# Kernel optimization log

Measured on AMD Instinct MI355X. Metric: run time of the kernel, lower is better.

Reference implementation:

```python
import jax, jax.numpy as jnp
import numpy as np

B, T = 4, 2048
IN_H, OUT_H = 4096, 4096   # in_hidden_size = output features, out_hidden_size = input features (torch F.linear quirk)
RANK = 1024


def setup_inputs() -> dict:
    key = jax.random.key(0)
    kx, ku, ks, kv, kb = jax.random.split(key, 5)
    x = jax.random.normal(kx, (B, T, OUT_H), dtype=jnp.float32)
    U = jax.random.normal(ku, (IN_H, RANK), dtype=jnp.float32) * 0.02
    S = jax.random.uniform(ks, (RANK,), dtype=jnp.float32)
    V = jax.random.normal(kv, (OUT_H, RANK), dtype=jnp.float32) * 0.02
    bias = jax.random.normal(kb, (IN_H,), dtype=jnp.float32) * 0.01
    return {"x": x, "U": U, "S": S, "V": V, "bias": bias}


def reference(x, U, S, V, bias):
    # Faithful to torch: M = U @ diag(S) @ V.T  (shape [in_hidden, out_hidden]);
    # F.linear(x, M, bias) = x @ M.T + bias, so x:[...,out_hidden] -> out:[...,in_hidden]
    M = (U * S) @ V.T                     # [IN_H, OUT_H]; (U*S) == U @ diag(S)
    return jnp.einsum('bto,io->bti', x, M) + bias
```

## Files before the change

### kernel.cpp

```cpp
#include <hip/hip_runtime.h>
#include <stdint.h>

typedef __attribute__((ext_vector_type(4))) float  floatx4;
typedef __attribute__((ext_vector_type(8))) short  short8;
typedef __attribute__((ext_vector_type(8))) __bf16 bf16x8;

__device__ __forceinline__ unsigned short f2bf(float f) {
  unsigned int u = __builtin_bit_cast(unsigned int, f);
  u += 0x7fffu + ((u >> 16) & 1u);
  return (unsigned short)(u >> 16);
}

typedef const __attribute__((address_space(1))) void* gptr_t;
typedef __attribute__((address_space(3))) void*       lptr_t;

__global__ __launch_bounds__(256) void prep_fused(
    const float* __restrict__ X, const float* __restrict__ V,
    const float* __restrict__ U, const float* __restrict__ S,
    unsigned short* __restrict__ Xb, unsigned short* __restrict__ Vt,
    unsigned short* __restrict__ Ub,
    int castBlocks, int transTotal, int transGX, int vrows, int vcols,
    unsigned int rankMask) {
  __shared__ float tile[32][33];
  int bid = blockIdx.x;
  int tid = threadIdx.x;
  if (bid < castBlocks) {
    size_t i = ((size_t)bid * 256 + tid) * 8;
    const floatx4* p = (const floatx4*)(X + i);
    floatx4 a = p[0], b = p[1];
    union { unsigned short us[8]; short8 v; } o;
    o.us[0] = f2bf(a[0]); o.us[1] = f2bf(a[1]); o.us[2] = f2bf(a[2]); o.us[3] = f2bf(a[3]);
    o.us[4] = f2bf(b[0]); o.us[5] = f2bf(b[1]); o.us[6] = f2bf(b[2]); o.us[7] = f2bf(b[3]);
    *(short8*)(Xb + i) = o.v;
  } else if (bid < castBlocks + transTotal) {
    int b  = bid - castBlocks;
    int bx = (b % transGX) * 32;
    int by = (b / transGX) * 32;
    int tx = tid & 31;
    int ty = tid >> 5;
    for (int i = ty; i < 32; i += 8)
      tile[i][tx] = V[(size_t)(by + i) * vcols + bx + tx];
    __syncthreads();
    for (int i = ty; i < 32; i += 8)
      Vt[(size_t)(bx + i) * vrows + by + tx] = f2bf(tile[tx][i]);
  } else {
    int b = bid - castBlocks - transTotal;
    size_t i = ((size_t)b * 256 + tid) * 4;
    floatx4 u = *(const floatx4*)(U + i);
    floatx4 s = *(const floatx4*)(S + (i & (size_t)rankMask));
    union { unsigned short us[4]; unsigned long long v; } o;
    o.us[0] = f2bf(u[0] * s[0]); o.us[1] = f2bf(u[1] * s[1]);
    o.us[2] = f2bf(u[2] * s[2]); o.us[3] = f2bf(u[3] * s[3]);
    *(unsigned long long*)(Ub + i) = o.v;
  }
}

__global__ __launch_bounds__(256, 2)
void gemm1_kernel(const unsigned short* __restrict__ A,
                  const unsigned short* __restrict__ Bt,
                  unsigned short* __restrict__ C,
                  int N, int K, int GX) {
  __shared__ unsigned short sA[2][128 * 32];
  __shared__ unsigned short sB[2][128 * 32];

  const int tid  = threadIdx.x;
  const int lane = tid & 63;
  const int wave = tid >> 6;
  const int wm = (wave >> 1) * 64;
  const int wn = (wave & 1) * 64;

  unsigned bid  = blockIdx.x;
  unsigned bw   = 8u * GX;
  unsigned band = bid / bw, rem = bid % bw;
  unsigned by   = band * 8 + (rem & 7u);
  unsigned bx   = rem >> 3;
  const int row0 = by * 128, col0 = bx * 128;

  floatx4 acc[4][4];
#pragma unroll
  for (int i = 0; i < 4; ++i)
#pragma unroll
    for (int j = 0; j < 4; ++j) acc[i][j] = (floatx4){0.f, 0.f, 0.f, 0.f};

  const unsigned short* Ablk = A + (size_t)row0 * K;
  const unsigned short* Bblk = Bt + (size_t)col0 * K;

  const int r0 = tid >> 2, c0 = (tid & 3) * 8;
  const int ldso0 = (wave * 64) * 8;
  const int ldso1 = (256 + wave * 64) * 8;
  const int mrow = lane & 15, quad = lane >> 4;

  for (int k0 = 0; k0 < K; k0 += 64) {
#pragma unroll
    for (int t = 0; t < 2; ++t) {
      const int kk = k0 + t * 32;
      __builtin_amdgcn_global_load_lds((gptr_t)(Ablk + (size_t)r0 * K + kk + c0),
                                       (lptr_t)(sA[t] + ldso0), 16, 0, 0);
      __builtin_amdgcn_global_load_lds((gptr_t)(Ablk + (size_t)(r0 + 64) * K + kk + c0),
                                       (lptr_t)(sA[t] + ldso1), 16, 0, 0);
      __builtin_amdgcn_global_load_lds((gptr_t)(Bblk + (size_t)r0 * K + kk + c0),
                                       (lptr_t)(sB[t] + ldso0), 16, 0, 0);
      __builtin_amdgcn_global_load_lds((gptr_t)(Bblk + (size_t)(r0 + 64) * K + kk + c0),
                                       (lptr_t)(sB[t] + ldso1), 16, 0, 0);
    }
    __syncthreads();
#pragma unroll
    for (int t = 0; t < 2; ++t) {
      bf16x8 af[4], bfr[4];
#pragma unroll
      for (int mi = 0; mi < 4; ++mi)
        af[mi] = __builtin_bit_cast(bf16x8,
                  *(const short8*)(sA[t] + (wm + mi * 16 + mrow) * 32 + quad * 8));
#pragma unroll
      for (int ni = 0; ni < 4; ++ni)
        bfr[ni] = __builtin_bit_cast(bf16x8,
                  *(const short8*)(sB[t] + (wn + ni * 16 + mrow) * 32 + quad * 8));
#pragma unroll
      for (int mi = 0; mi < 4; ++mi)
#pragma unroll
        for (int ni = 0; ni < 4; ++ni)
          acc[mi][ni] = __builtin_amdgcn_mfma_f32_16x16x32_bf16(af[mi], bfr[ni],
                                                                acc[mi][ni], 0, 0, 0);
    }
    __syncthreads();
  }

  const int orow = row0 + wm + quad * 4;
  const int ocol = col0 + wn + mrow;
#pragma unroll
  for (int mi = 0; mi < 4; ++mi)
#pragma unroll
    for (int r = 0; r < 4; ++r) {
      size_t rowoff = (size_t)(orow + mi * 16 + r) * N;
#pragma unroll
      for (int ni = 0; ni < 4; ++ni)
        C[rowoff + ocol + ni * 16] = f2bf(acc[mi][ni][r]);
    }
}

__global__ __launch_bounds__(512, 2)
void gemm2_kernel(const unsigned short* __restrict__ A,
                  const unsigned short* __restrict__ Bt,
                  float* __restrict__ C, const float* __restrict__ bias,
                  int N, int K, int GX) {
  __shared__ unsigned short sA[2][256 * 64];
  __shared__ unsigned short sB[2][256 * 64];

  const int tid  = threadIdx.x;
  const int lane = tid & 63;
  const int wave = tid >> 6;
  const int wm = (wave >> 2) * 128;
  const int wn = (wave & 3) * 64;

  unsigned bid  = blockIdx.x;
  unsigned bw   = 8u * GX;
  unsigned band = bid / bw, rem = bid % bw;
  unsigned by   = band * 8 + (rem & 7u);
  unsigned bx   = rem >> 3;
  const int row0 = by * 256, col0 = bx * 256;

  floatx4 acc[8][4];
#pragma unroll
  for (int i = 0; i < 8; ++i)
#pragma unroll
    for (int j = 0; j < 4; ++j) acc[i][j] = (floatx4){0.f, 0.f, 0.f, 0.f};

  const int srow = wave * 8 + (lane >> 3);
  const int ssl  = (lane & 7) ^ (lane >> 3);
  const unsigned short* Ag = A  + (size_t)(row0 + srow) * K + ssl * 8;
  const unsigned short* Bg = Bt + (size_t)(col0 + srow) * K + ssl * 8;
  const int ldsw = (wave * 8) * 64;

  const int mrow = lane & 15, quad = lane >> 4;
  const int sw = mrow & 7;
  const int paof[2] = { (wm + mrow) * 64 + ((quad ^ sw) << 3),
                        (wm + mrow) * 64 + (((quad + 4) ^ sw) << 3) };
  const int pbof[2] = { (wn + mrow) * 64 + ((quad ^ sw) << 3),
                        (wn + mrow) * 64 + (((quad + 4) ^ sw) << 3) };

  const int NKT = K >> 6;

#define STAGE_G2(KOFF, BUF)                                                    \
  {                                                                            \
    const unsigned short* As_ = Ag + (KOFF);                                   \
    const unsigned short* Bs_ = Bg + (KOFF);                                   \
    unsigned short* dA_ = &sA[(BUF)][0] + ldsw;                                \
    unsigned short* dB_ = &sB[(BUF)][0] + ldsw;                                \
    _Pragma("unroll")                                                          \
    for (int j_ = 0; j_ < 4; ++j_) {                                           \
      __builtin_amdgcn_global_load_lds((gptr_t)(As_ + (size_t)j_ * 64 * K),    \
                                       (lptr_t)(dA_ + j_ * 4096), 16, 0, 0);   \
      __builtin_amdgcn_global_load_lds((gptr_t)(Bs_ + (size_t)j_ * 64 * K),    \
                                       (lptr_t)(dB_ + j_ * 4096), 16, 0, 0);   \
    }                                                                          \
  }

  STAGE_G2(0, 0);
  STAGE_G2(64, 1);
  asm volatile("s_waitcnt vmcnt(8)" ::: "memory");
  __builtin_amdgcn_s_barrier();

  int cur = 0;
  for (int kt = 0; kt < NKT; ++kt) {
    const unsigned short* bA = &sA[cur][0];
    const unsigned short* bB = &sB[cur][0];
#pragma unroll
    for (int ks = 0; ks < 2; ++ks) {
      bf16x8 bfr[4], af[8];
#pragma unroll
      for (int ni = 0; ni < 4; ++ni)
        bfr[ni] = __builtin_bit_cast(bf16x8,
                    *(const short8*)(bB + pbof[ks] + ni * 1024));
#pragma unroll
      for (int mi = 0; mi < 8; ++mi)
        af[mi] = __builtin_bit_cast(bf16x8,
                    *(const short8*)(bA + paof[ks] + mi * 1024));
      __builtin_amdgcn_s_setprio(1);
#pragma unroll
      for (int mi = 0; mi < 8; ++mi)
#pragma unroll
        for (int ni = 0; ni < 4; ++ni)
          acc[mi][ni] = __builtin_amdgcn_mfma_f32_16x16x32_bf16(af[mi], bfr[ni],
                                                                acc[mi][ni], 0, 0, 0);
      __builtin_amdgcn_s_setprio(0);
    }
    asm volatile("s_waitcnt lgkmcnt(0)" ::: "memory");
    __builtin_amdgcn_sched_barrier(0);
    __builtin_amdgcn_s_barrier();
    __builtin_amdgcn_sched_barrier(0);
    if (kt + 2 < NKT) {
      STAGE_G2((kt + 2) * 64, cur);
      asm volatile("s_waitcnt vmcnt(8)" ::: "memory");
      __builtin_amdgcn_s_barrier();
    } else if (kt + 1 < NKT) {
      asm volatile("s_waitcnt vmcnt(0)" ::: "memory");
      __builtin_amdgcn_s_barrier();
    }
    cur ^= 1;
  }
#undef STAGE_G2

  const int orow = row0 + wm + quad * 4;
  const int ocol = col0 + wn + mrow;
  float bv[4];
#pragma unroll
  for (int ni = 0; ni < 4; ++ni) bv[ni] = bias[ocol + ni * 16];
#pragma unroll
  for (int mi = 0; mi < 8; ++mi)
#pragma unroll
    for (int r = 0; r < 4; ++r) {
      size_t rowoff = (size_t)(orow + mi * 16 + r) * N;
#pragma unroll
      for (int ni = 0; ni < 4; ++ni)
        C[rowoff + ocol + ni * 16] = acc[mi][ni][r] + bv[ni];
    }
}

extern "C" void kernel_launch(void* const* d_in, const int* in_sizes, int n_in,
                              void* d_out, int out_size, void* d_ws, size_t ws_size,
                              hipStream_t stream) {
  const float* x    = (const float*)d_in[0];
  const float* U    = (const float*)d_in[1];
  const float* S    = (const float*)d_in[2];
  const float* V    = (const float*)d_in[3];
  const float* bias = (const float*)d_in[4];

  const int RANK = in_sizes[2];
  const int INH  = in_sizes[4];
  const int OUTH = in_sizes[3] / RANK;
  const int M    = in_sizes[0] / OUTH;

  unsigned short* Xb = (unsigned short*)d_ws;
  unsigned short* Vt = Xb + (size_t)M * OUTH;
  unsigned short* Ub = Vt + (size_t)RANK * OUTH;
  unsigned short* Yb = Ub + (size_t)INH * RANK;

  const int castBlocks = (int)(((size_t)M * OUTH) / 2048);
  const int transGX    = RANK / 32;
  const int transTotal = transGX * (OUTH / 32);
  const int prepUBlk   = (int)(((size_t)INH * RANK) / 1024);
  prep_fused<<<castBlocks + transTotal + prepUBlk, 256, 0, stream>>>(
      x, V, U, S, Xb, Vt, Ub, castBlocks, transTotal, transGX, OUTH, RANK,
      (unsigned)(RANK - 1));

  gemm1_kernel<<<(M / 128) * (RANK / 128), 256, 0, stream>>>(
      Xb, Vt, Yb, RANK, OUTH, RANK / 128);

  gemm2_kernel<<<(M / 256) * (INH / 256), 512, 0, stream>>>(
      Yb, Ub, (float*)d_out, bias, INH, RANK, INH / 256);
}
```

Before: 397.8 us.

## Split GEMM K-step into two half-tile phases with interleaved partial LDS staging

Restructures the main bf16 MFMA loop so each K-tile is processed in two phases, first the upper four M-subtiles and then the lower four. Global-to-LDS loads are split into two groups: A rows 64/192, and A rows 0/128 plus all of B. Each group is issued between phases with its own vmcnt waits and barriers. The aim is to overlap global loads and LDS reads with MFMA work more finely and to cut register pressure from holding all A fragments at once. The cost is more barriers per iteration and a tricky ordering of buffer reuse that could race if the vmcnt accounting is wrong.

```diff
diff --git a/kernel.cpp b/kernel.cpp
--- a/kernel.cpp
+++ b/kernel.cpp
@@ -172,73 +172,111 @@
   const int ldsw = (wave * 8) * 64;
 
   const int mrow = lane & 15, quad = lane >> 4;
-  const int sw = mrow & 7;
-  const int paof[2] = { (wm + mrow) * 64 + ((quad ^ sw) << 3),
-                        (wm + mrow) * 64 + (((quad + 4) ^ sw) << 3) };
-  const int pbof[2] = { (wn + mrow) * 64 + ((quad ^ sw) << 3),
-                        (wn + mrow) * 64 + (((quad + 4) ^ sw) << 3) };
+  const int sw   = mrow & 7;
+  const int pko0 = ((quad    ) ^ sw) << 3;
+  const int pko1 = ((quad + 4) ^ sw) << 3;
 
   const int NKT = K >> 6;
 
-#define STAGE_G2(KOFF, BUF)                                                    \
+#define STAGE_RA1(BUF, KOFF)                                                   \
+  {                                                                            \
+    const unsigned short* As_ = Ag + (KOFF);                                   \
+    unsigned short* dA_ = &sA[(BUF)][0] + ldsw;                                \
+    __builtin_amdgcn_global_load_lds((gptr_t)(As_ + (size_t)64 * K),           \
+                                     (lptr_t)(dA_ + 4096), 16, 0, 0);          \
+    __builtin_amdgcn_global_load_lds((gptr_t)(As_ + (size_t)192 * K),          \
+                                     (lptr_t)(dA_ + 12288), 16, 0, 0);         \
+  }
+
+#define STAGE_RA0RB(BUF, KOFF)                                                 \
   {                                                                            \
     const unsigned short* As_ = Ag + (KOFF);                                   \
     const unsigned short* Bs_ = Bg + (KOFF);                                   \
     unsigned short* dA_ = &sA[(BUF)][0] + ldsw;                                \
     unsigned short* dB_ = &sB[(BUF)][0] + ldsw;                                \
+    __builtin_amdgcn_global_load_lds((gptr_t)(As_),                            \
+                                     (lptr_t)(dA_), 16, 0, 0);                 \
+    __builtin_amdgcn_global_load_lds((gptr_t)(As_ + (size_t)128 * K),          \
+                                     (lptr_t)(dA_ + 8192), 16, 0, 0);          \
     _Pragma("unroll")                                                          \
-    for (int j_ = 0; j_ < 4; ++j_) {                                           \
-      __builtin_amdgcn_global_load_lds((gptr_t)(As_ + (size_t)j_ * 64 * K),    \
-                                       (lptr_t)(dA_ + j_ * 4096), 16, 0, 0);   \
+    for (int j_ = 0; j_ < 4; ++j_)                                             \
       __builtin_amdgcn_global_load_lds((gptr_t)(Bs_ + (size_t)j_ * 64 * K),    \
                                        (lptr_t)(dB_ + j_ * 4096), 16, 0, 0);   \
-    }                                                                          \
-  }
-
-  STAGE_G2(0, 0);
-  STAGE_G2(64, 1);
-  asm volatile("s_waitcnt vmcnt(8)" ::: "memory");
-  __builtin_amdgcn_s_barrier();
-
-  int cur = 0;
+  }
+
+  STAGE_RA0RB(0, 0);
+  STAGE_RA1 (0, 0);
+  STAGE_RA0RB(1, 64);
+
   for (int kt = 0; kt < NKT; ++kt) {
-    const unsigned short* bA = &sA[cur][0];
-    const unsigned short* bB = &sB[cur][0];
-#pragma unroll
-    for (int ks = 0; ks < 2; ++ks) {
-      bf16x8 bfr[4], af[8];
-#pragma unroll
-      for (int ni = 0; ni < 4; ++ni)
-        bfr[ni] = __builtin_bit_cast(bf16x8,
-                    *(const short8*)(bB + pbof[ks] + ni * 1024));
-#pragma unroll
-      for (int mi = 0; mi < 8; ++mi)
-        af[mi] = __builtin_bit_cast(bf16x8,
-                    *(const short8*)(bA + paof[ks] + mi * 1024));
-      __builtin_amdgcn_s_setprio(1);
-#pragma unroll
-      for (int mi = 0; mi < 8; ++mi)
+    const int c = kt & 1;
+    const unsigned short* bA = &sA[c][0];
+    const unsigned short* bB = &sB[c][0];
+
+    asm volatile("s_waitcnt vmcnt(8)" ::: "memory");
+    __builtin_amdgcn_sched_barrier(0);
+    if (kt + 1 < NKT) STAGE_RA1(c ^ 1, (kt + 1) * 64);
+    bf16x8 b0[4][2], a0[4][2];
+#pragma unroll
+    for (int ni = 0; ni < 4; ++ni) {
+      const unsigned short* p = bB + (wn + ni * 16 + mrow) * 64;
+      b0[ni][0] = __builtin_bit_cast(bf16x8, *(const short8*)(p + pko0));
+      b0[ni][1] = __builtin_bit_cast(bf16x8, *(const short8*)(p + pko1));
+    }
+#pragma unroll
+    for (int i = 0; i < 4; ++i) {
+      const unsigned short* p = bA + (wm + i * 16 + mrow) * 64;
+      a0[i][0] = __builtin_bit_cast(bf16x8, *(const short8*)(p + pko0));
+      a0[i][1] = __builtin_bit_cast(bf16x8, *(const short8*)(p + pko1));
+    }
+    __builtin_amdgcn_sched_barrier(0);
+    __builtin_amdgcn_s_barrier();
+    asm volatile("s_waitcnt lgkmcnt(0)" ::: "memory");
+    __builtin_amdgcn_sched_barrier(0);
+    __builtin_amdgcn_s_setprio(1);
+#pragma unroll
+    for (int ks = 0; ks < 2; ++ks)
+#pragma unroll
+      for (int i = 0; i < 4; ++i)
 #pragma unroll
         for (int ni = 0; ni < 4; ++ni)
-          acc[mi][ni] = __builtin_amdgcn_mfma_f32_16x16x32_bf16(af[mi], bfr[ni],
-                                                                acc[mi][ni], 0, 0, 0);
-      __builtin_amdgcn_s_setprio(0);
-    }
+          acc[i][ni] = __builtin_amdgcn_mfma_f32_16x16x32_bf16(a0[i][ks], b0[ni][ks],
+                                                               acc[i][ni], 0, 0, 0);
+    __builtin_amdgcn_s_setprio(0);
+    __builtin_amdgcn_s_barrier();
+
+    if (kt + 2 < NKT) {
+      asm volatile("s_waitcnt vmcnt(8)" ::: "memory");
+    } else {
+      asm volatile("s_waitcnt vmcnt(0)" ::: "memory");
+    }
+    __builtin_amdgcn_sched_barrier(0);
+    if (kt + 2 < NKT) STAGE_RA0RB(c, (kt + 2) * 64);
+    bf16x8 a1[4][2];
+#pragma unroll
+    for (int i = 0; i < 4; ++i) {
+      const unsigned short* p = bA + (wm + 64 + i * 16 + mrow) * 64;
+      a1[i][0] = __builtin_bit_cast(bf16x8, *(const short8*)(p + pko0));
+      a1[i][1] = __builtin_bit_cast(bf16x8, *(const short8*)(p + pko1));
+    }
+    __builtin_amdgcn_sched_barrier(0);
+    __builtin_amdgcn_s_barrier();
     asm volatile("s_waitcnt lgkmcnt(0)" ::: "memory");
     __builtin_amdgcn_sched_barrier(0);
+    __builtin_amdgcn_s_setprio(1);
+#pragma unroll
+    for (int ks = 0; ks < 2; ++ks)
+#pragma unroll
+      for (int i = 0; i < 4; ++i)
+#pragma unroll
+        for (int ni = 0; ni < 4; ++ni)
+          acc[4 + i][ni] = __builtin_amdgcn_mfma_f32_16x16x32_bf16(a1[i][ks], b0[ni][ks],
+                                                                   acc[4 + i][ni], 0, 0, 0);
+    __builtin_amdgcn_s_setprio(0);
     __builtin_amdgcn_s_barrier();
-    __builtin_amdgcn_sched_barrier(0);
-    if (kt + 2 < NKT) {
-      STAGE_G2((kt + 2) * 64, cur);
-      asm volatile("s_waitcnt vmcnt(8)" ::: "memory");
-      __builtin_amdgcn_s_barrier();
-    } else if (kt + 1 < NKT) {
-      asm volatile("s_waitcnt vmcnt(0)" ::: "memory");
-      __builtin_amdgcn_s_barrier();
-    }
-    cur ^= 1;
-  }
-#undef STAGE_G2
+  }
+#undef STAGE_RA1
+#undef STAGE_RA0RB
 
   const int orow = row0 + wm + quad * 4;
   const int ocol = col0 + wn + mrow;
```

After: 418.3 us. +5.2%, slower.

## Double-buffer gemm1 K-tiles with XOR-swizzled LDS and prefetch overlap

Applied to the files above, without the earlier changes.

Reworks the gemm1 main loop into a two-stage pipeline. Each stage loads a full 64-wide K slab into its own LDS buffer, and the next-but-one tile is prefetched while the current one is computed. Partial vmcnt waits replace the full syncthreads, and an XOR swizzle on LDS columns is meant to avoid bank conflicts on the fragment reads. MFMA sections are bracketed with setprio to favour math issue. LDS use doubles, which may affect occupancy, and the hand-written waitcnt and barrier logic is delicate.

```diff
diff --git a/kernel.cpp b/kernel.cpp
--- a/kernel.cpp
+++ b/kernel.cpp
@@ -60,8 +60,8 @@
                   const unsigned short* __restrict__ Bt,
                   unsigned short* __restrict__ C,
                   int N, int K, int GX) {
-  __shared__ unsigned short sA[2][128 * 32];
-  __shared__ unsigned short sB[2][128 * 32];
+  __shared__ unsigned short sA[2][128 * 64];
+  __shared__ unsigned short sB[2][128 * 64];
 
   const int tid  = threadIdx.x;
   const int lane = tid & 63;
@@ -82,48 +82,79 @@
 #pragma unroll
     for (int j = 0; j < 4; ++j) acc[i][j] = (floatx4){0.f, 0.f, 0.f, 0.f};
 
-  const unsigned short* Ablk = A + (size_t)row0 * K;
-  const unsigned short* Bblk = Bt + (size_t)col0 * K;
-
-  const int r0 = tid >> 2, c0 = (tid & 3) * 8;
-  const int ldso0 = (wave * 64) * 8;
-  const int ldso1 = (256 + wave * 64) * 8;
+  const int srow = wave * 8 + (lane >> 3);
+  const int ssl  = (lane & 7) ^ (lane >> 3);
+  const unsigned short* Ag = A  + (size_t)(row0 + srow) * K + ssl * 8;
+  const unsigned short* Bg = Bt + (size_t)(col0 + srow) * K + ssl * 8;
+  const int ldsw = (wave * 8) * 64;
+
   const int mrow = lane & 15, quad = lane >> 4;
-
-  for (int k0 = 0; k0 < K; k0 += 64) {
-#pragma unroll
-    for (int t = 0; t < 2; ++t) {
-      const int kk = k0 + t * 32;
-      __builtin_amdgcn_global_load_lds((gptr_t)(Ablk + (size_t)r0 * K + kk + c0),
-                                       (lptr_t)(sA[t] + ldso0), 16, 0, 0);
-      __builtin_amdgcn_global_load_lds((gptr_t)(Ablk + (size_t)(r0 + 64) * K + kk + c0),
-                                       (lptr_t)(sA[t] + ldso1), 16, 0, 0);
-      __builtin_amdgcn_global_load_lds((gptr_t)(Bblk + (size_t)r0 * K + kk + c0),
-                                       (lptr_t)(sB[t] + ldso0), 16, 0, 0);
-      __builtin_amdgcn_global_load_lds((gptr_t)(Bblk + (size_t)(r0 + 64) * K + kk + c0),
-                                       (lptr_t)(sB[t] + ldso1), 16, 0, 0);
-    }
-    __syncthreads();
-#pragma unroll
-    for (int t = 0; t < 2; ++t) {
-      bf16x8 af[4], bfr[4];
+  const int sw   = mrow & 7;
+  const int pko0 = ((quad    ) ^ sw) << 3;
+  const int pko1 = ((quad + 4) ^ sw) << 3;
+
+  const int NKT = K >> 6;
+
+#define STAGE_G1(KOFF, BUF)                                                    \
+  {                                                                            \
+    const unsigned short* As_ = Ag + (KOFF);                                   \
+    const unsigned short* Bs_ = Bg + (KOFF);                                   \
+    unsigned short* dA_ = &sA[(BUF)][0] + ldsw;                                \
+    unsigned short* dB_ = &sB[(BUF)][0] + ldsw;                                \
+    _Pragma("unroll")                                                          \
+    for (int j_ = 0; j_ < 4; ++j_) {                                           \
+      __builtin_amdgcn_global_load_lds((gptr_t)(As_ + (size_t)j_ * 32 * K),    \
+                                       (lptr_t)(dA_ + j_ * 2048), 16, 0, 0);   \
+      __builtin_amdgcn_global_load_lds((gptr_t)(Bs_ + (size_t)j_ * 32 * K),    \
+                                       (lptr_t)(dB_ + j_ * 2048), 16, 0, 0);   \
+    }                                                                          \
+  }
+
+  STAGE_G1(0, 0);
+  STAGE_G1(64, 1);
+  asm volatile("s_waitcnt vmcnt(8)" ::: "memory");
+  __builtin_amdgcn_s_barrier();
+
+  int cur = 0;
+  for (int kt = 0; kt < NKT; ++kt) {
+    const unsigned short* bA = &sA[cur][0];
+    const unsigned short* bB = &sB[cur][0];
+#pragma unroll
+    for (int ks = 0; ks < 2; ++ks) {
+      const int pko = ks ? pko1 : pko0;
+      bf16x8 bfr[4], af[4];
+#pragma unroll
+      for (int ni = 0; ni < 4; ++ni)
+        bfr[ni] = __builtin_bit_cast(bf16x8,
+                    *(const short8*)(bB + (wn + ni * 16 + mrow) * 64 + pko));
 #pragma unroll
       for (int mi = 0; mi < 4; ++mi)
         af[mi] = __builtin_bit_cast(bf16x8,
-                  *(const short8*)(sA[t] + (wm + mi * 16 + mrow) * 32 + quad * 8));
-#pragma unroll
-      for (int ni = 0; ni < 4; ++ni)
-        bfr[ni] = __builtin_bit_cast(bf16x8,
-                  *(const short8*)(sB[t] + (wn + ni * 16 + mrow) * 32 + quad * 8));
+                    *(const short8*)(bA + (wm + mi * 16 + mrow) * 64 + pko));
+      __builtin_amdgcn_s_setprio(1);
 #pragma unroll
       for (int mi = 0; mi < 4; ++mi)
 #pragma unroll
         for (int ni = 0; ni < 4; ++ni)
           acc[mi][ni] = __builtin_amdgcn_mfma_f32_16x16x32_bf16(af[mi], bfr[ni],
                                                                 acc[mi][ni], 0, 0, 0);
-    }
-    __syncthreads();
-  }
+      __builtin_amdgcn_s_setprio(0);
+    }
+    asm volatile("s_waitcnt lgkmcnt(0)" ::: "memory");
+    __builtin_amdgcn_sched_barrier(0);
+    __builtin_amdgcn_s_barrier();
+    __builtin_amdgcn_sched_barrier(0);
+    if (kt + 2 < NKT) {
+      STAGE_G1((kt + 2) * 64, cur);
+      asm volatile("s_waitcnt vmcnt(8)" ::: "memory");
+      __builtin_amdgcn_s_barrier();
+    } else if (kt + 1 < NKT) {
+      asm volatile("s_waitcnt vmcnt(0)" ::: "memory");
+      __builtin_amdgcn_s_barrier();
+    }
+    cur ^= 1;
+  }
+#undef STAGE_G1
 
   const int orow = row0 + wm + quad * 4;
   const int ocol = col0 + wn + mrow;
```

Measured after the change: 391.4 us. Within noise of the previous version (-1.6%).
